# Kernel optimization log

Measured on AMD Instinct MI355X. Metric: run time of the kernel, lower is better.

Reference implementation:

```python
import jax, jax.numpy as jnp
import numpy as np

B, C = 16, 1024
EPS = 1e-12
TINY = 1e-9


def setup_inputs() -> dict:
    key = jax.random.key(0)
    k1, k2 = jax.random.split(key)
    lower = jax.random.normal(k1, (B, C), dtype=jnp.float32)
    # guarantee upper >= lower as required by bound propagation
    upper = lower + jax.random.uniform(k2, (B, C), dtype=jnp.float32)
    return {"lower": lower, "upper": upper}


def reference(lower, upper):
    l, u = lower, upper
    Bv, Cv = l.shape
    eye = jnp.eye(Cv, dtype=l.dtype)          # (C,C)
    offdiag = 1.0 - eye                        # zero on diagonal

    # pairwise logit differences d_ij = x_j - x_i, bounded by [l_d, u_d]; diag forced to 0
    l_d = (l[:, None, :] - u[:, :, None]) * offdiag   # (B,C,C)
    u_d = (u[:, None, :] - l[:, :, None]) * offdiag   # (B,C,C)

    exp_l = jnp.exp(l_d)
    exp_u = jnp.exp(u_d)

    # exp upper bound: secant over [l_d, u_d]
    denom = u_d - l_d
    a_u = (exp_u - exp_l) / (denom + EPS)
    a_u = jnp.where(jnp.abs(denom) < TINY, exp_u, a_u)
    b_u = exp_l - a_u * l_d

    # exp lower bound: tangent at midpoint t
    t = 0.5 * (l_d + u_d)
    a_l = jnp.exp(t)
    b_l = a_l - a_l * t                        # exp(t) - a_l * t

    # zero diagonal entries (i == j term excluded from the sum)
    a_u = a_u * offdiag
    b_u = b_u * offdiag
    a_l = a_l * offdiag
    b_l = b_l * offdiag
    exp_l_od = exp_l * offdiag
    exp_u_od = exp_u * offdiag

    S_l = exp_l_od.sum(axis=2)                 # (B,C)
    S_u = exp_u_od.sum(axis=2)                 # (B,C)

    # linear coefficients of S_i w.r.t. logits x: off-diag from a, diag collects -sum_j a_ij
    sum_a_u = a_u.sum(axis=2)                  # (B,C)
    sum_a_l = a_l.sum(axis=2)
    coef_S_upper = a_u - eye[None, :, :] * sum_a_u[:, :, None]
    coef_S_lower = a_l - eye[None, :, :] * sum_a_l[:, :, None]
    bias_S_upper = b_u.sum(axis=2)
    bias_S_lower = b_l.sum(axis=2)

    # g(S) = 1 / (1 + S), decreasing & convex
    g_at_S_l = 1.0 / (1.0 + S_l)
    g_at_S_u = 1.0 / (1.0 + S_u)

    # upper relaxation of g: tangent (secant of decreasing convex fn swaps roles)
    denom_g = S_u - S_l
    m_u = (g_at_S_u - g_at_S_l) / (denom_g + EPS)
    m_u = jnp.where(jnp.abs(denom_g) < TINY, -1.0 / (1.0 + S_u) ** 2, m_u)
    c_u = g_at_S_l - m_u * S_l

    # lower relaxation of g: tangent at S_u
    m_l = -1.0 / (1.0 + S_u) ** 2
    c_l = 1.0 / (1.0 + S_u) - m_l * S_u

    # compose (m_u >= ... careful with sign handled as in original: direct product)
    final_upper_coef = m_u[:, :, None] * coef_S_upper   # (B,C,C)
    final_lower_coef = m_l[:, :, None] * coef_S_lower   # (B,C,C)
    final_upper_bias = m_u * bias_S_upper + c_u          # (B,C)
    final_lower_bias = m_l * bias_S_lower + c_l          # (B,C)

    soft_lower = jnp.clip(g_at_S_u, 0.0, 1.0)
    soft_upper = jnp.clip(g_at_S_l, 0.0, 1.0)

    return (soft_lower, soft_upper,
            final_lower_coef, final_upper_coef,
            final_lower_bias, final_upper_bias)
```

## Files before the change

### kernel.cpp

```cpp
#include <hip/hip_runtime.h>

namespace {

constexpr int B = 16;
constexpr int C = 1024;
constexpr int BC = B * C;
constexpr long long BCC = (long long)B * C * C;
constexpr float EPS  = 1e-12f;
constexpr float TINY = 1e-9f;

__global__ __launch_bounds__(256) void bounded_softmax_kernel(
    const float* __restrict__ lower,
    const float* __restrict__ upper,
    float* __restrict__ out)
{
    const int row = blockIdx.x;
    const int b   = row >> 10;
    const int i   = row & (C - 1);
    const int tid = threadIdx.x;

    const float* __restrict__ lrow = lower + b * C;
    const float* __restrict__ urow = upper + b * C;

    const float l_i = lrow[i];
    const float u_i = urow[i];

    const float4 lj4 = *reinterpret_cast<const float4*>(lrow + tid * 4);
    const float4 uj4 = *reinterpret_cast<const float4*>(urow + tid * 4);
    const float ljv[4] = {lj4.x, lj4.y, lj4.z, lj4.w};
    const float ujv[4] = {uj4.x, uj4.y, uj4.z, uj4.w};

    float a_u[4], a_l[4];
    float acc[6] = {0.f, 0.f, 0.f, 0.f, 0.f, 0.f};

    #pragma unroll
    for (int k = 0; k < 4; ++k) {
        const int j = tid * 4 + k;
        const float l_d = ljv[k] - u_i;
        const float u_d = ujv[k] - l_i;
        const float el  = __expf(l_d);
        const float eu  = __expf(u_d);
        const float denom = u_d - l_d;
        float au = (eu - el) / (denom + EPS);
        au = (fabsf(denom) < TINY) ? eu : au;
        const float bu = fmaf(-au, l_d, el);
        const float t  = 0.5f * (l_d + u_d);
        const float al = __expf(t);
        const float bl = al * (1.0f - t);

        float elz = el, euz = eu, auz = au, buz = bu, alz = al, blz = bl;
        if (j == i) { elz = euz = auz = buz = alz = blz = 0.0f; }

        acc[0] += elz; acc[1] += euz; acc[2] += auz;
        acc[3] += alz; acc[4] += buz; acc[5] += blz;
        a_u[k] = auz; a_l[k] = alz;
    }

    __shared__ float red[4][6];
    const int lane = tid & 63;
    const int wid  = tid >> 6;
    #pragma unroll
    for (int m = 0; m < 6; ++m) {
        float v = acc[m];
        #pragma unroll
        for (int o = 32; o > 0; o >>= 1) v += __shfl_down(v, o);
        if (lane == 0) red[wid][m] = v;
    }
    __syncthreads();

    const float S_l  = red[0][0] + red[1][0] + red[2][0] + red[3][0];
    const float S_u  = red[0][1] + red[1][1] + red[2][1] + red[3][1];
    const float SA_u = red[0][2] + red[1][2] + red[2][2] + red[3][2];
    const float SA_l = red[0][3] + red[1][3] + red[2][3] + red[3][3];
    const float SB_u = red[0][4] + red[1][4] + red[2][4] + red[3][4];
    const float SB_l = red[0][5] + red[1][5] + red[2][5] + red[3][5];

    const float g_l = 1.0f / (1.0f + S_l);
    const float g_u = 1.0f / (1.0f + S_u);
    const float dg  = S_u - S_l;
    float m_u = (g_u - g_l) / (dg + EPS);
    m_u = (fabsf(dg) < TINY) ? (-g_u * g_u) : m_u;
    const float c_u = g_l - m_u * S_l;
    const float m_l = -g_u * g_u;
    const float c_l = g_u - m_l * S_u;

    float* __restrict__ lower_coef = out + 2 * BC + (long long)row * C;
    float* __restrict__ upper_coef = out + 2 * BC + BCC + (long long)row * C;

    float lv[4], uv[4];
    #pragma unroll
    for (int k = 0; k < 4; ++k) {
        const int j = tid * 4 + k;
        const float dl = (j == i) ? SA_l : 0.0f;
        const float du = (j == i) ? SA_u : 0.0f;
        lv[k] = m_l * (a_l[k] - dl);
        uv[k] = m_u * (a_u[k] - du);
    }
    *reinterpret_cast<float4*>(lower_coef + tid * 4) =
        make_float4(lv[0], lv[1], lv[2], lv[3]);
    *reinterpret_cast<float4*>(upper_coef + tid * 4) =
        make_float4(uv[0], uv[1], uv[2], uv[3]);

    if (tid == 0) {
        const float soft_lower = fminf(fmaxf(g_u, 0.0f), 1.0f);
        const float soft_upper = fminf(fmaxf(g_l, 0.0f), 1.0f);
        out[row]                          = soft_lower;
        out[BC + row]                     = soft_upper;
        out[2 * BC + 2 * BCC + row]       = fmaf(m_l, SB_l, c_l);
        out[2 * BC + 2 * BCC + BC + row]  = fmaf(m_u, SB_u, c_u);
    }
}

}

extern "C" void kernel_launch(void* const* d_in, const int* in_sizes, int n_in,
                              void* d_out, int out_size, void* d_ws, size_t ws_size,
                              hipStream_t stream) {
    const float* lower = (const float*)d_in[0];
    const float* upper = (const float*)d_in[1];
    float* out = (float*)d_out;
    bounded_softmax_kernel<<<dim3(B * C), dim3(256), 0, stream>>>(lower, upper, out);
}
```

Measured before the change: 149.9 us.

## Factor pairwise exps into per-element exp products via precompute kernel

Uses exp(x_j - x_i) = exp(x_j)/exp(x_i) to replace the three per-pair exponentials with multiplications by precomputed per-element exps. A separate small kernel writes those exps to the workspace. Other changes: the secant divide becomes a hardware reciprocal, the diagonal masking moves into a separate correction loop, and the coefficient writes become nontemporal stores. The risks are overflow or underflow for large logits, lower accuracy from rcp, and an extra kernel launch plus workspace reads.

```diff
diff --git a/kernel.cpp b/kernel.cpp
--- a/kernel.cpp
+++ b/kernel.cpp
@@ -9,9 +9,27 @@
 constexpr float EPS  = 1e-12f;
 constexpr float TINY = 1e-9f;
 
+typedef float vfloat4 __attribute__((ext_vector_type(4)));
+
+__global__ __launch_bounds__(256) void precompute_exps(
+    const float* __restrict__ lower,
+    const float* __restrict__ upper,
+    float* __restrict__ El, float* __restrict__ Eu, float* __restrict__ Em)
+{
+    const int idx = blockIdx.x * 256 + threadIdx.x;
+    const float l = lower[idx];
+    const float u = upper[idx];
+    El[idx] = __expf(l);
+    Eu[idx] = __expf(u);
+    Em[idx] = __expf(0.5f * (l + u));
+}
+
 __global__ __launch_bounds__(256) void bounded_softmax_kernel(
     const float* __restrict__ lower,
     const float* __restrict__ upper,
+    const float* __restrict__ El,
+    const float* __restrict__ Eu,
+    const float* __restrict__ Em,
     float* __restrict__ out)
 {
     const int row = blockIdx.x;
@@ -21,39 +39,69 @@
 
     const float* __restrict__ lrow = lower + b * C;
     const float* __restrict__ urow = upper + b * C;
+    const float* __restrict__ Elr  = El + b * C;
+    const float* __restrict__ Eur  = Eu + b * C;
+    const float* __restrict__ Emr  = Em + b * C;
 
     const float l_i = lrow[i];
     const float u_i = urow[i];
+    const float s_el = __builtin_amdgcn_rcpf(Eur[i]);
+    const float s_eu = __builtin_amdgcn_rcpf(Elr[i]);
+    const float s_em = __builtin_amdgcn_rcpf(Emr[i]);
 
-    const float4 lj4 = *reinterpret_cast<const float4*>(lrow + tid * 4);
-    const float4 uj4 = *reinterpret_cast<const float4*>(urow + tid * 4);
-    const float ljv[4] = {lj4.x, lj4.y, lj4.z, lj4.w};
-    const float ujv[4] = {uj4.x, uj4.y, uj4.z, uj4.w};
+    const float4 l4  = *reinterpret_cast<const float4*>(lrow + tid * 4);
+    const float4 u4  = *reinterpret_cast<const float4*>(urow + tid * 4);
+    const float4 El4 = *reinterpret_cast<const float4*>(Elr + tid * 4);
+    const float4 Eu4 = *reinterpret_cast<const float4*>(Eur + tid * 4);
+    const float4 Em4 = *reinterpret_cast<const float4*>(Emr + tid * 4);
+    const float ljv[4] = {l4.x, l4.y, l4.z, l4.w};
+    const float ujv[4] = {u4.x, u4.y, u4.z, u4.w};
+    const float Elv[4] = {El4.x, El4.y, El4.z, El4.w};
+    const float Euv[4] = {Eu4.x, Eu4.y, Eu4.z, Eu4.w};
+    const float Emv[4] = {Em4.x, Em4.y, Em4.z, Em4.w};
 
     float a_u[4], a_l[4];
     float acc[6] = {0.f, 0.f, 0.f, 0.f, 0.f, 0.f};
 
     #pragma unroll
     for (int k = 0; k < 4; ++k) {
-        const int j = tid * 4 + k;
         const float l_d = ljv[k] - u_i;
         const float u_d = ujv[k] - l_i;
-        const float el  = __expf(l_d);
-        const float eu  = __expf(u_d);
+        const float el  = Elv[k] * s_el;
+        const float eu  = Euv[k] * s_eu;
+        const float am  = Emv[k] * s_em;
         const float denom = u_d - l_d;
-        float au = (eu - el) / (denom + EPS);
-        au = (fabsf(denom) < TINY) ? eu : au;
-        const float bu = fmaf(-au, l_d, el);
+        const float r  = __builtin_amdgcn_rcpf(denom + EPS);
+        float a = (eu - el) * r;
+        a = (fabsf(denom) < TINY) ? eu : a;
+        const float bu = fmaf(-a, l_d, el);
         const float t  = 0.5f * (l_d + u_d);
-        const float al = __expf(t);
-        const float bl = al * (1.0f - t);
+        const float bl = fmaf(-am, t, am);
 
-        float elz = el, euz = eu, auz = au, buz = bu, alz = al, blz = bl;
-        if (j == i) { elz = euz = auz = buz = alz = blz = 0.0f; }
+        acc[0] += el; acc[1] += eu; acc[2] += a;
+        acc[3] += am; acc[4] += bu; acc[5] += bl;
+        a_u[k] = a; a_l[k] = am;
+    }
 
-        acc[0] += elz; acc[1] += euz; acc[2] += auz;
-        acc[3] += alz; acc[4] += buz; acc[5] += blz;
-        a_u[k] = auz; a_l[k] = alz;
+    #pragma unroll
+    for (int k = 0; k < 4; ++k) {
+        if (tid * 4 + k == i) {
+            const float l_d = ljv[k] - u_i;
+            const float u_d = ujv[k] - l_i;
+            const float el  = Elv[k] * s_el;
+            const float eu  = Euv[k] * s_eu;
+            const float am  = Emv[k] * s_em;
+            const float denom = u_d - l_d;
+            const float r  = __builtin_amdgcn_rcpf(denom + EPS);
+            float a = (eu - el) * r;
+            a = (fabsf(denom) < TINY) ? eu : a;
+            const float bu = fmaf(-a, l_d, el);
+            const float t  = 0.5f * (l_d + u_d);
+            const float bl = fmaf(-am, t, am);
+            acc[0] -= el; acc[1] -= eu; acc[2] -= a;
+            acc[3] -= am; acc[4] -= bu; acc[5] -= bl;
+            a_u[k] = 0.0f; a_l[k] = 0.0f;
+        }
     }
 
     __shared__ float red[4][6];
@@ -87,19 +135,15 @@
     float* __restrict__ lower_coef = out + 2 * BC + (long long)row * C;
     float* __restrict__ upper_coef = out + 2 * BC + BCC + (long long)row * C;
 
-    float lv[4], uv[4];
+    vfloat4 lv, uv;
     #pragma unroll
     for (int k = 0; k < 4; ++k) {
-        const int j = tid * 4 + k;
-        const float dl = (j == i) ? SA_l : 0.0f;
-        const float du = (j == i) ? SA_u : 0.0f;
-        lv[k] = m_l * (a_l[k] - dl);
-        uv[k] = m_u * (a_u[k] - du);
+        const bool diag = (tid * 4 + k == i);
+        lv[k] = m_l * (diag ? -SA_l : a_l[k]);
+        uv[k] = m_u * (diag ? -SA_u : a_u[k]);
     }
-    *reinterpret_cast<float4*>(lower_coef + tid * 4) =
-        make_float4(lv[0], lv[1], lv[2], lv[3]);
-    *reinterpret_cast<float4*>(upper_coef + tid * 4) =
-        make_float4(uv[0], uv[1], uv[2], uv[3]);
+    __builtin_nontemporal_store(lv, reinterpret_cast<vfloat4*>(lower_coef + tid * 4));
+    __builtin_nontemporal_store(uv, reinterpret_cast<vfloat4*>(upper_coef + tid * 4));
 
     if (tid == 0) {
         const float soft_lower = fminf(fmaxf(g_u, 0.0f), 1.0f);
@@ -119,5 +163,9 @@
     const float* lower = (const float*)d_in[0];
     const float* upper = (const float*)d_in[1];
     float* out = (float*)d_out;
-    bounded_softmax_kernel<<<dim3(B * C), dim3(256), 0, stream>>>(lower, upper, out);
+    float* El = (float*)d_ws;
+    float* Eu = El + BC;
+    float* Em = Eu + BC;
+    precompute_exps<<<dim3(BC / 256), dim3(256), 0, stream>>>(lower, upper, El, Eu, Em);
+    bounded_softmax_kernel<<<dim3(BC), dim3(256), 0, stream>>>(lower, upper, El, Eu, Em, out);
 }
```

After: 155.3 us. +3.6%, slower.
